# Optimization experiments

Measured on AMD Instinct MI355X. Metric: run time of the kernel, lower is better.

The kernel has to match this reference:

```python
import math
import jax, jax.numpy as jnp
import numpy as np

B, L, H = 32, 1024, 128

def setup_inputs() -> dict:
    key = jax.random.key(0)
    k1, k2, k3, k4 = jax.random.split(key, 4)
    a = jax.random.normal(k1, (B, L, H), dtype=jnp.float32)
    b = jax.random.normal(k2, (B, L, H), dtype=jnp.float32)
    mask_a = jax.random.randint(k3, (B, L, 1), 0, 2, dtype=jnp.int32)
    mask_b = jax.random.randint(k4, (B, L, 1), 0, 2, dtype=jnp.int32)
    temperature = jnp.asarray(1.0 / math.sqrt(H), dtype=jnp.float32)
    return {"a": a, "b": b, "mask_a": mask_a, "mask_b": mask_b, "temperature": temperature}

def reference(a, b, mask_a, mask_b, temperature):
    # scores: [B, La, Lb]
    scores = jnp.einsum('bld,bmd->blm', a, b) * temperature
    # outer product of token validity masks -> pair mask [B, La, Lb]
    mask = jnp.einsum('blk,bmk->blm', mask_a.astype(jnp.float32), mask_b.astype(jnp.float32)) > 0
    scores = jnp.where(mask, scores, jnp.float32(-10000.0))
    attention_a = jax.nn.softmax(scores, axis=1)  # normalize over La (columns)
    attention_b = jax.nn.softmax(scores, axis=2)  # normalize over Lb (rows)
    feature_a = jnp.einsum('blm,bmd->bld', attention_b, b)
    feature_b = jnp.einsum('blm,bmd->bld', attention_a, a)  # valid since La == Lb
    return (feature_a, feature_b)
```

## Files before the change

kernel.cpp:

```cpp
#include <hip/hip_runtime.h>
#include <math.h>

#define BN 32
#define LL 1024
#define HH 128

typedef __attribute__((ext_vector_type(8))) short short8;
typedef __attribute__((ext_vector_type(4))) float f32x4;

static const size_t SZ_BF = (size_t)BN * LL * HH * 2;

__device__ __forceinline__ ushort f2bf(float x) {
  union { float f; unsigned u; } c; c.f = x;
  unsigned r = c.u + 0x7fffu + ((c.u >> 16) & 1u);
  return (ushort)(r >> 16);
}
__device__ __forceinline__ float bf2f(ushort h) {
  union { unsigned u; float f; } c; c.u = ((unsigned)h) << 16;
  return c.f;
}
__device__ __forceinline__ short8 ld8(const ushort* p) {
  return *(const short8*)p;
}

__global__ __launch_bounds__(256) void k_convert(
    const float* __restrict__ a, const float* __restrict__ b,
    const int* __restrict__ mask_b,
    ushort* __restrict__ abf, ushort* __restrict__ bbf,
    ushort* __restrict__ aT, ushort* __restrict__ bT,
    float* __restrict__ meanb, float* __restrict__ invmean) {
  int bb = blockIdx.y;
  int l0 = blockIdx.x * 64;
  int which = blockIdx.z;
  const float* src = which ? b : a;
  ushort* dst  = which ? bbf : abf;
  ushort* dstT = which ? bT : aT;
  float* dmean = which ? meanb : invmean;
  __shared__ __align__(16) ushort T[128][72];
  __shared__ float accS[128];
  __shared__ float wgt[64];
  int t = threadIdx.x;
  if (t < 128) accS[t] = 0.f;
  if (t < 64)
    wgt[t] = which ? 1.0f : ((mask_b[bb * LL + l0 + t] == 0) ? 1.0f : 0.0f);
  int lrow = t >> 5;
  int dcol = (t & 31) * 4;
#pragma unroll
  for (int p = 0; p < 8; ++p) {
    int l = p * 8 + lrow;
    float4 v = *(const float4*)&src[((size_t)bb * LL + l0 + l) * HH + dcol];
    ushort4 u;
    u.x = f2bf(v.x); u.y = f2bf(v.y); u.z = f2bf(v.z); u.w = f2bf(v.w);
    *(ushort4*)&dst[((size_t)bb * LL + l0 + l) * HH + dcol] = u;
    T[dcol + 0][l] = u.x; T[dcol + 1][l] = u.y;
    T[dcol + 2][l] = u.z; T[dcol + 3][l] = u.w;
  }
  __syncthreads();
  int drow = t >> 3;
  int c8 = (t & 7) * 8;
#pragma unroll
  for (int q = 0; q < 4; ++q) {
    int d = q * 32 + drow;
    short8 val = *(const short8*)&T[d][c8];
    *(short8*)&dstT[((size_t)bb * HH + d) * LL + l0 + c8] = val;
    float s = 0.f;
#pragma unroll
    for (int j = 0; j < 8; ++j) s += wgt[c8 + j] * bf2f((ushort)val[j]);
    atomicAdd(&accS[d], s);
  }
  __syncthreads();
  if (t < 128) atomicAdd(&dmean[bb * HH + t], accS[t]);
}

__global__ __launch_bounds__(256, 2) void k_colsum(
    const ushort* __restrict__ abf, const ushort* __restrict__ bbf,
    const int* __restrict__ mask_a, const int* __restrict__ mask_b,
    const float* __restrict__ temp_p, float2* __restrict__ cc) {
  int bb = blockIdx.y;
  int m0 = blockIdx.x * 64;
  int t = threadIdx.x;
  int w = t >> 6, lane = t & 63, l16 = lane & 15, quad = lane >> 4;
  float temp = temp_p[0];
  __shared__ __align__(16) float biasA[LL];
  __shared__ float csred[4][4][16];
  for (int i = t; i < LL; i += 256)
    biasA[i] = mask_a[bb * LL + i] ? 0.0f : -10000.0f;

  short8 Bm[4][4];
  float biasB_mt[4];
#pragma unroll
  for (int mt = 0; mt < 4; ++mt) {
    int m = m0 + mt * 16 + l16;
    biasB_mt[mt] = mask_b[bb * LL + m] ? 0.0f : -10000.0f;
#pragma unroll
    for (int k = 0; k < 4; ++k)
      Bm[mt][k] = ld8(&bbf[((size_t)bb * LL + m) * HH + k * 32 + quad * 8]);
  }
  __syncthreads();

  float cs[4] = {0.f, 0.f, 0.f, 0.f};
  short8 Al0[4], Al1[4];

#define LOADAL(AlX, IT)                                                       \
  {                                                                           \
    const ushort* arow = &abf[((size_t)bb * LL + w * 256 + (IT) * 16 + l16) * HH]; \
    _Pragma("unroll") for (int k = 0; k < 4; ++k)                             \
        AlX[k] = ld8(&arow[k * 32 + quad * 8]);                               \
  }

#define CSCOMPUTE(AlX, IT)                                                    \
  {                                                                           \
    int lbase = w * 256 + (IT) * 16;                                          \
    f32x4 bA = *(const f32x4*)&biasA[lbase + quad * 4];                       \
    _Pragma("unroll") for (int mt = 0; mt < 4; ++mt) {                        \
      f32x4 sacc = {0.f, 0.f, 0.f, 0.f};                                      \
      _Pragma("unroll") for (int k = 0; k < 4; ++k)                           \
          sacc = __builtin_amdgcn_mfma_f32_16x16x32_bf16(AlX[k], Bm[mt][k],   \
                                                         sacc, 0, 0, 0);      \
      _Pragma("unroll") for (int r = 0; r < 4; ++r)                           \
          cs[mt] += __expf(sacc[r] * temp + bA[r] + biasB_mt[mt]);            \
    }                                                                         \
  }

  LOADAL(Al0, 0);
  for (int it = 0; it < 16; it += 2) {
    LOADAL(Al1, it + 1);
    CSCOMPUTE(Al0, it);
    LOADAL(Al0, (it + 2) & 15);
    CSCOMPUTE(Al1, it + 1);
  }
#undef LOADAL
#undef CSCOMPUTE

#pragma unroll
  for (int mt = 0; mt < 4; ++mt) {
    cs[mt] += __shfl_xor(cs[mt], 16);
    cs[mt] += __shfl_xor(cs[mt], 32);
  }
  if (lane < 16) {
#pragma unroll
    for (int mt = 0; mt < 4; ++mt) csred[w][mt][l16] = cs[mt];
  }
  __syncthreads();
  if (t < 64) {
    int mt = t >> 4, ml = t & 15;
    float s = csred[0][mt][ml] + csred[1][mt][ml] + csred[2][mt][ml] + csred[3][mt][ml];
    int m = m0 + t;
    float bB = mask_b[bb * LL + m] ? 0.0f : -10000.0f;
    cc[bb * LL + m] = make_float2(s > 0.f ? 1.0f / s : 0.0f, bB);
  }
}

__global__ __launch_bounds__(256, 2) void k_features(
    const ushort* __restrict__ abf, const ushort* __restrict__ bbf,
    const ushort* __restrict__ aT, const ushort* __restrict__ bT,
    const int* __restrict__ mask_a, const float* __restrict__ temp_p,
    const float2* __restrict__ cc, const float* __restrict__ meanb,
    const float* __restrict__ invmean, float* __restrict__ out) {
  int bb = blockIdx.y;
  int l0 = blockIdx.x * 64;
  int t = threadIdx.x;
  int w = t >> 6, lane = t & 63, l16 = lane & 15, quad = lane >> 4;
  float temp = temp_p[0];

  __shared__ float2 ccs[LL];
  __shared__ __align__(16) ushort Pa[2][64 * 72];
  __shared__ __align__(16) ushort Pb[2][64 * 72];
  __shared__ float rspart[4][64];
  __shared__ float rsfin[64];

  for (int i = t; i < LL; i += 256) ccs[i] = cc[bb * LL + i];

  float biasA_lt[4];
  short8 Afix[4][4];
#pragma unroll
  for (int lt = 0; lt < 4; ++lt) {
    int l = l0 + lt * 16 + l16;
    biasA_lt[lt] = mask_a[bb * LL + l] ? 0.0f : -10000.0f;
#pragma unroll
    for (int k = 0; k < 4; ++k)
      Afix[lt][k] = ld8(&abf[((size_t)bb * LL + l) * HH + k * 32 + quad * 8]);
  }

  f32x4 accA[4][2], accB[4][2];
  f32x4 zero = {0.f, 0.f, 0.f, 0.f};
#pragma unroll
  for (int lt = 0; lt < 4; ++lt)
#pragma unroll
    for (int dt = 0; dt < 2; ++dt) { accA[lt][dt] = zero; accB[lt][dt] = zero; }
  float rs_lt[4] = {0.f, 0.f, 0.f, 0.f};
  __syncthreads();

  short8 Am0[4], Am1[4];
  float2 cv0[4], cv1[4];
  short8 Bb[2][2], Ba[2][2];

#define LOADAM(AmX, cvX, M0)                                                  \
  {                                                                           \
    const ushort* brow = &bbf[((size_t)bb * LL + (M0) + w * 16 + l16) * HH];  \
    _Pragma("unroll") for (int k = 0; k < 4; ++k)                             \
        AmX[k] = ld8(&brow[k * 32 + quad * 8]);                               \
    _Pragma("unroll") for (int r = 0; r < 4; ++r)                             \
        cvX[r] = ccs[(M0) + w * 16 + quad * 4 + r];                           \
  }

#define LOADBT(M0)                                                            \
  {                                                                           \
    _Pragma("unroll") for (int dt = 0; dt < 2; ++dt) {                        \
      const ushort* btrow =                                                   \
          &bT[((size_t)bb * HH + w * 32 + dt * 16 + l16) * LL + (M0)];        \
      const ushort* atrow =                                                   \
          &aT[((size_t)bb * HH + w * 32 + dt * 16 + l16) * LL + (M0)];        \
      _Pragma("unroll") for (int ks = 0; ks < 2; ++ks) {                      \
        Bb[dt][ks] = ld8(&btrow[ks * 32 + quad * 8]);                         \
        Ba[dt][ks] = ld8(&atrow[ks * 32 + quad * 8]);                         \
      }                                                                       \
    }                                                                         \
  }

#define SPHASE(AmX, cvX)                                                      \
  {                                                                           \
    ushort* pa = &Pa[buf][0];                                                 \
    ushort* pb = &Pb[buf][0];                                                 \
    _Pragma("unroll") for (int lt = 0; lt < 4; ++lt) {                        \
      f32x4 sacc = zero;                                                      \
      _Pragma("unroll") for (int k = 0; k < 4; ++k)                           \
          sacc = __builtin_amdgcn_mfma_f32_16x16x32_bf16(AmX[k], Afix[lt][k], \
                                                         sacc, 0, 0, 0);      \
      ushort pav[4], pbv[4];                                                  \
      _Pragma("unroll") for (int r = 0; r < 4; ++r) {                         \
        float e = __expf(sacc[r] * temp + biasA_lt[lt] + cvX[r].y);           \
        pav[r] = f2bf(e);                                                     \
        rs_lt[lt] += bf2f(pav[r]);                                            \
        pbv[r] = f2bf(e * cvX[r].x);                                          \
      }                                                                       \
      uint2 ka, kb;                                                           \
      ka.x = (uint)pav[0] | ((uint)pav[1] << 16);                             \
      ka.y = (uint)pav[2] | ((uint)pav[3] << 16);                             \
      kb.x = (uint)pbv[0] | ((uint)pbv[1] << 16);                             \
      kb.y = (uint)pbv[2] | ((uint)pbv[3] << 16);                             \
      int pidx = (lt * 16 + l16) * 72 + w * 16 + quad * 4;                    \
      *(uint2*)&pa[pidx] = ka;                                                \
      *(uint2*)&pb[pidx] = kb;                                                \
    }                                                                         \
  }

#define FPHASE()                                                              \
  {                                                                           \
    const ushort* pa = &Pa[buf][0];                                           \
    const ushort* pb = &Pb[buf][0];                                           \
    _Pragma("unroll") for (int lt = 0; lt < 4; ++lt) {                        \
      _Pragma("unroll") for (int ks = 0; ks < 2; ++ks) {                      \
        int ridx = (lt * 16 + l16) * 72 + ks * 32 + quad * 8;                 \
        short8 PaF = *(const short8*)&pa[ridx];                               \
        short8 PbF = *(const short8*)&pb[ridx];                               \
        _Pragma("unroll") for (int dt = 0; dt < 2; ++dt) {                    \
          accA[lt][dt] = __builtin_amdgcn_mfma_f32_16x16x32_bf16(             \
              PaF, Bb[dt][ks], accA[lt][dt], 0, 0, 0);                        \
          accB[lt][dt] = __builtin_amdgcn_mfma_f32_16x16x32_bf16(             \
              PbF, Ba[dt][ks], accB[lt][dt], 0, 0, 0);                        \
        }                                                                     \
      }                                                                       \
    }                                                                         \
  }

  LOADAM(Am0, cv0, 0);
  int buf = 0;
  for (int m0 = 0; m0 < LL; m0 += 128) {
    LOADBT(m0);
    LOADAM(Am1, cv1, m0 + 64);
    SPHASE(Am0, cv0);
    __syncthreads();
    FPHASE();
    buf ^= 1;
    LOADBT(m0 + 64);
    LOADAM(Am0, cv0, (m0 + 128) & (LL - 1));
    SPHASE(Am1, cv1);
    __syncthreads();
    FPHASE();
    buf ^= 1;
  }
#undef LOADAM
#undef LOADBT
#undef SPHASE
#undef FPHASE

#pragma unroll
  for (int lt = 0; lt < 4; ++lt) {
    rs_lt[lt] += __shfl_xor(rs_lt[lt], 16);
    rs_lt[lt] += __shfl_xor(rs_lt[lt], 32);
  }
  if (lane < 16) {
#pragma unroll
    for (int lt = 0; lt < 4; ++lt) rspart[w][lt * 16 + l16] = rs_lt[lt];
  }
  __syncthreads();
  if (t < 64)
    rsfin[t] = rspart[0][t] + rspart[1][t] + rspart[2][t] + rspart[3][t];
  __syncthreads();

  float* outA = out;
  float* outB = out + (size_t)BN * LL * HH;
#pragma unroll
  for (int dt = 0; dt < 2; ++dt) {
    int d = w * 32 + dt * 16 + l16;
    float mb = meanb[bb * HH + d] * (1.0f / 1024.0f);
    float im = invmean[bb * HH + d] * (1.0f / 1024.0f);
#pragma unroll
    for (int lt = 0; lt < 4; ++lt) {
#pragma unroll
      for (int r = 0; r < 4; ++r) {
        int l = lt * 16 + quad * 4 + r;
        float rsv = rsfin[l];
        float fa = (rsv > 0.f) ? accA[lt][dt][r] / rsv : mb;
        float fb = accB[lt][dt][r] + im;
        outA[((size_t)bb * LL + l0 + l) * HH + d] = fa;
        outB[((size_t)bb * LL + l0 + l) * HH + d] = fb;
      }
    }
  }
}

extern "C" void kernel_launch(void* const* d_in, const int* in_sizes, int n_in,
                              void* d_out, int out_size, void* d_ws, size_t ws_size,
                              hipStream_t stream) {
  const float* a = (const float*)d_in[0];
  const float* b = (const float*)d_in[1];
  const int* mask_a = (const int*)d_in[2];
  const int* mask_b = (const int*)d_in[3];
  const float* temp = (const float*)d_in[4];
  float* out = (float*)d_out;

  char* wsb = (char*)d_ws;
  ushort* abf = (ushort*)(wsb + 0 * SZ_BF);
  ushort* bbf = (ushort*)(wsb + 1 * SZ_BF);
  ushort* aT  = (ushort*)(wsb + 2 * SZ_BF);
  ushort* bT  = (ushort*)(wsb + 3 * SZ_BF);
  float2* cc  = (float2*)(wsb + 4 * SZ_BF);
  float* meanb   = (float*)(wsb + 4 * SZ_BF + (size_t)BN * LL * sizeof(float2));
  float* invmean = meanb + BN * HH;

  hipMemsetAsync(meanb, 0, 2 * BN * HH * sizeof(float), stream);
  k_convert<<<dim3(16, 32, 2), 256, 0, stream>>>(a, b, mask_b, abf, bbf, aT, bT,
                                                 meanb, invmean);
  k_colsum<<<dim3(16, 32), 256, 0, stream>>>(abf, bbf, mask_a, mask_b, temp, cc);
  k_features<<<dim3(16, 32), 256, 0, stream>>>(abf, bbf, aT, bT, mask_a, temp,
                                               cc, meanb, invmean, out);
  (void)in_sizes; (void)n_in; (void)out_size; (void)ws_size;
}
```

Baseline: 206.7 us.

## Halve row tile to 32, move fixed A fragments to LDS, drop software prefetch

Both the column-sum and feature kernels now handle 32 rows per block instead of 64, doubling the grid to 1024 blocks and raising the launch-bounds occupancy hint from 2 to 4 waves per SIMD. In the feature kernel the fixed A fragments move from registers into shared memory, and the double-buffered register prefetch of B/A tiles is replaced by a simple per-iteration load. This cuts register pressure so more waves can hide latency. The cost is twice the re-reading of B and the transposed tiles across blocks, less MFMA work per load, and no explicit load/compute overlap.

```diff
diff --git a/kernel.cpp b/kernel.cpp
--- a/kernel.cpp
+++ b/kernel.cpp
@@ -72,24 +72,24 @@
   if (t < 128) atomicAdd(&dmean[bb * HH + t], accS[t]);
 }
 
-__global__ __launch_bounds__(256, 2) void k_colsum(
+__global__ __launch_bounds__(256, 4) void k_colsum(
     const ushort* __restrict__ abf, const ushort* __restrict__ bbf,
     const int* __restrict__ mask_a, const int* __restrict__ mask_b,
     const float* __restrict__ temp_p, float2* __restrict__ cc) {
   int bb = blockIdx.y;
-  int m0 = blockIdx.x * 64;
+  int m0 = blockIdx.x * 32;
   int t = threadIdx.x;
   int w = t >> 6, lane = t & 63, l16 = lane & 15, quad = lane >> 4;
   float temp = temp_p[0];
   __shared__ __align__(16) float biasA[LL];
-  __shared__ float csred[4][4][16];
+  __shared__ float csred[4][2][16];
   for (int i = t; i < LL; i += 256)
     biasA[i] = mask_a[bb * LL + i] ? 0.0f : -10000.0f;
 
-  short8 Bm[4][4];
-  float biasB_mt[4];
-#pragma unroll
-  for (int mt = 0; mt < 4; ++mt) {
+  short8 Bm[2][4];
+  float biasB_mt[2];
+#pragma unroll
+  for (int mt = 0; mt < 2; ++mt) {
     int m = m0 + mt * 16 + l16;
     biasB_mt[mt] = mask_b[bb * LL + m] ? 0.0f : -10000.0f;
 #pragma unroll
@@ -98,7 +98,7 @@
   }
   __syncthreads();
 
-  float cs[4] = {0.f, 0.f, 0.f, 0.f};
+  float cs[2] = {0.f, 0.f};
   short8 Al0[4], Al1[4];
 
 #define LOADAL(AlX, IT)                                                       \
@@ -112,7 +112,7 @@
   {                                                                           \
     int lbase = w * 256 + (IT) * 16;                                          \
     f32x4 bA = *(const f32x4*)&biasA[lbase + quad * 4];                       \
-    _Pragma("unroll") for (int mt = 0; mt < 4; ++mt) {                        \
+    _Pragma("unroll") for (int mt = 0; mt < 2; ++mt) {                        \
       f32x4 sacc = {0.f, 0.f, 0.f, 0.f};                                      \
       _Pragma("unroll") for (int k = 0; k < 4; ++k)                           \
           sacc = __builtin_amdgcn_mfma_f32_16x16x32_bf16(AlX[k], Bm[mt][k],   \
@@ -133,16 +133,16 @@
 #undef CSCOMPUTE
 
 #pragma unroll
-  for (int mt = 0; mt < 4; ++mt) {
+  for (int mt = 0; mt < 2; ++mt) {
     cs[mt] += __shfl_xor(cs[mt], 16);
     cs[mt] += __shfl_xor(cs[mt], 32);
   }
   if (lane < 16) {
 #pragma unroll
-    for (int mt = 0; mt < 4; ++mt) csred[w][mt][l16] = cs[mt];
-  }
-  __syncthreads();
-  if (t < 64) {
+    for (int mt = 0; mt < 2; ++mt) csred[w][mt][l16] = cs[mt];
+  }
+  __syncthreads();
+  if (t < 32) {
     int mt = t >> 4, ml = t & 15;
     float s = csred[0][mt][ml] + csred[1][mt][ml] + csred[2][mt][ml] + csred[3][mt][ml];
     int m = m0 + t;
@@ -151,151 +151,131 @@
   }
 }
 
-__global__ __launch_bounds__(256, 2) void k_features(
+__global__ __launch_bounds__(256, 4) void k_features(
     const ushort* __restrict__ abf, const ushort* __restrict__ bbf,
     const ushort* __restrict__ aT, const ushort* __restrict__ bT,
     const int* __restrict__ mask_a, const float* __restrict__ temp_p,
     const float2* __restrict__ cc, const float* __restrict__ meanb,
     const float* __restrict__ invmean, float* __restrict__ out) {
   int bb = blockIdx.y;
-  int l0 = blockIdx.x * 64;
+  int l0 = blockIdx.x * 32;
   int t = threadIdx.x;
   int w = t >> 6, lane = t & 63, l16 = lane & 15, quad = lane >> 4;
   float temp = temp_p[0];
 
   __shared__ float2 ccs[LL];
-  __shared__ __align__(16) ushort Pa[2][64 * 72];
-  __shared__ __align__(16) ushort Pb[2][64 * 72];
-  __shared__ float rspart[4][64];
-  __shared__ float rsfin[64];
+  __shared__ __align__(16) ushort Pa[2][32 * 72];
+  __shared__ __align__(16) ushort Pb[2][32 * 72];
+  __shared__ short8 AfixS[512];
+  __shared__ float rspart[4][32];
+  __shared__ float rsfin[32];
 
   for (int i = t; i < LL; i += 256) ccs[i] = cc[bb * LL + i];
 
-  float biasA_lt[4];
-  short8 Afix[4][4];
-#pragma unroll
-  for (int lt = 0; lt < 4; ++lt) {
+  {
+    int l16p = t & 15, quadp = (t >> 4) & 3, kp = t >> 6;
+#pragma unroll
+    for (int lt = 0; lt < 2; ++lt) {
+      short8 v = ld8(&abf[((size_t)bb * LL + l0 + lt * 16 + l16p) * HH +
+                          kp * 32 + quadp * 8]);
+      AfixS[((lt * 4 + kp) * 4 + quadp) * 16 + l16p] = v;
+    }
+  }
+
+  float biasA_lt[2];
+#pragma unroll
+  for (int lt = 0; lt < 2; ++lt) {
     int l = l0 + lt * 16 + l16;
     biasA_lt[lt] = mask_a[bb * LL + l] ? 0.0f : -10000.0f;
-#pragma unroll
-    for (int k = 0; k < 4; ++k)
-      Afix[lt][k] = ld8(&abf[((size_t)bb * LL + l) * HH + k * 32 + quad * 8]);
-  }
-
-  f32x4 accA[4][2], accB[4][2];
+  }
+
+  f32x4 accA[2][2], accB[2][2];
   f32x4 zero = {0.f, 0.f, 0.f, 0.f};
 #pragma unroll
-  for (int lt = 0; lt < 4; ++lt)
+  for (int lt = 0; lt < 2; ++lt)
 #pragma unroll
     for (int dt = 0; dt < 2; ++dt) { accA[lt][dt] = zero; accB[lt][dt] = zero; }
-  float rs_lt[4] = {0.f, 0.f, 0.f, 0.f};
-  __syncthreads();
-
-  short8 Am0[4], Am1[4];
-  float2 cv0[4], cv1[4];
-  short8 Bb[2][2], Ba[2][2];
-
-#define LOADAM(AmX, cvX, M0)                                                  \
-  {                                                                           \
-    const ushort* brow = &bbf[((size_t)bb * LL + (M0) + w * 16 + l16) * HH];  \
-    _Pragma("unroll") for (int k = 0; k < 4; ++k)                             \
-        AmX[k] = ld8(&brow[k * 32 + quad * 8]);                               \
-    _Pragma("unroll") for (int r = 0; r < 4; ++r)                             \
-        cvX[r] = ccs[(M0) + w * 16 + quad * 4 + r];                           \
-  }
-
-#define LOADBT(M0)                                                            \
-  {                                                                           \
-    _Pragma("unroll") for (int dt = 0; dt < 2; ++dt) {                        \
-      const ushort* btrow =                                                   \
-          &bT[((size_t)bb * HH + w * 32 + dt * 16 + l16) * LL + (M0)];        \
-      const ushort* atrow =                                                   \
-          &aT[((size_t)bb * HH + w * 32 + dt * 16 + l16) * LL + (M0)];        \
-      _Pragma("unroll") for (int ks = 0; ks < 2; ++ks) {                      \
-        Bb[dt][ks] = ld8(&btrow[ks * 32 + quad * 8]);                         \
-        Ba[dt][ks] = ld8(&atrow[ks * 32 + quad * 8]);                         \
-      }                                                                       \
-    }                                                                         \
-  }
-
-#define SPHASE(AmX, cvX)                                                      \
-  {                                                                           \
-    ushort* pa = &Pa[buf][0];                                                 \
-    ushort* pb = &Pb[buf][0];                                                 \
-    _Pragma("unroll") for (int lt = 0; lt < 4; ++lt) {                        \
-      f32x4 sacc = zero;                                                      \
-      _Pragma("unroll") for (int k = 0; k < 4; ++k)                           \
-          sacc = __builtin_amdgcn_mfma_f32_16x16x32_bf16(AmX[k], Afix[lt][k], \
-                                                         sacc, 0, 0, 0);      \
-      ushort pav[4], pbv[4];                                                  \
-      _Pragma("unroll") for (int r = 0; r < 4; ++r) {                         \
-        float e = __expf(sacc[r] * temp + biasA_lt[lt] + cvX[r].y);           \
-        pav[r] = f2bf(e);                                                     \
-        rs_lt[lt] += bf2f(pav[r]);                                            \
-        pbv[r] = f2bf(e * cvX[r].x);                                          \
-      }                                                                       \
-      uint2 ka, kb;                                                           \
-      ka.x = (uint)pav[0] | ((uint)pav[1] << 16);                             \
-      ka.y = (uint)pav[2] | ((uint)pav[3] << 16);                             \
-      kb.x = (uint)pbv[0] | ((uint)pbv[1] << 16);                             \
-      kb.y = (uint)pbv[2] | ((uint)pbv[3] << 16);                             \
-      int pidx = (lt * 16 + l16) * 72 + w * 16 + quad * 4;                    \
-      *(uint2*)&pa[pidx] = ka;                                                \
-      *(uint2*)&pb[pidx] = kb;                                                \
-    }                                                                         \
-  }
-
-#define FPHASE()                                                              \
-  {                                                                           \
-    const ushort* pa = &Pa[buf][0];                                           \
-    const ushort* pb = &Pb[buf][0];                                           \
-    _Pragma("unroll") for (int lt = 0; lt < 4; ++lt) {                        \
-      _Pragma("unroll") for (int ks = 0; ks < 2; ++ks) {                      \
-        int ridx = (lt * 16 + l16) * 72 + ks * 32 + quad * 8;                 \
-        short8 PaF = *(const short8*)&pa[ridx];                               \
-        short8 PbF = *(const short8*)&pb[ridx];                               \
-        _Pragma("unroll") for (int dt = 0; dt < 2; ++dt) {                    \
-          accA[lt][dt] = __builtin_amdgcn_mfma_f32_16x16x32_bf16(             \
-              PaF, Bb[dt][ks], accA[lt][dt], 0, 0, 0);                        \
-          accB[lt][dt] = __builtin_amdgcn_mfma_f32_16x16x32_bf16(             \
-              PbF, Ba[dt][ks], accB[lt][dt], 0, 0, 0);                        \
-        }                                                                     \
-      }                                                                       \
-    }                                                                         \
-  }
-
-  LOADAM(Am0, cv0, 0);
+  float rs_lt[2] = {0.f, 0.f};
+  __syncthreads();
+
   int buf = 0;
-  for (int m0 = 0; m0 < LL; m0 += 128) {
-    LOADBT(m0);
-    LOADAM(Am1, cv1, m0 + 64);
-    SPHASE(Am0, cv0);
+  for (int mq = 0; mq < LL; mq += 64) {
+    short8 Am[4];
+    const ushort* brow = &bbf[((size_t)bb * LL + mq + w * 16 + l16) * HH];
+#pragma unroll
+    for (int k = 0; k < 4; ++k) Am[k] = ld8(&brow[k * 32 + quad * 8]);
+    short8 Bb[2][2], Ba[2][2];
+#pragma unroll
+    for (int dt = 0; dt < 2; ++dt) {
+      const ushort* btrow = &bT[((size_t)bb * HH + w * 32 + dt * 16 + l16) * LL + mq];
+      const ushort* atrow = &aT[((size_t)bb * HH + w * 32 + dt * 16 + l16) * LL + mq];
+#pragma unroll
+      for (int ks = 0; ks < 2; ++ks) {
+        Bb[dt][ks] = ld8(&btrow[ks * 32 + quad * 8]);
+        Ba[dt][ks] = ld8(&atrow[ks * 32 + quad * 8]);
+      }
+    }
+    float2 cv[4];
+#pragma unroll
+    for (int r = 0; r < 4; ++r) cv[r] = ccs[mq + w * 16 + quad * 4 + r];
+
+    ushort* pa = &Pa[buf][0];
+    ushort* pb = &Pb[buf][0];
+#pragma unroll
+    for (int lt = 0; lt < 2; ++lt) {
+      f32x4 sacc = zero;
+#pragma unroll
+      for (int k = 0; k < 4; ++k) {
+        short8 af = AfixS[((lt * 4 + k) * 4 + quad) * 16 + l16];
+        sacc = __builtin_amdgcn_mfma_f32_16x16x32_bf16(Am[k], af, sacc, 0, 0, 0);
+      }
+      ushort pav[4], pbv[4];
+#pragma unroll
+      for (int r = 0; r < 4; ++r) {
+        float e = __expf(sacc[r] * temp + biasA_lt[lt] + cv[r].y);
+        pav[r] = f2bf(e);
+        rs_lt[lt] += bf2f(pav[r]);
+        pbv[r] = f2bf(e * cv[r].x);
+      }
+      uint2 ka, kb;
+      ka.x = (uint)pav[0] | ((uint)pav[1] << 16);
+      ka.y = (uint)pav[2] | ((uint)pav[3] << 16);
+      kb.x = (uint)pbv[0] | ((uint)pbv[1] << 16);
+      kb.y = (uint)pbv[2] | ((uint)pbv[3] << 16);
+      int pidx = (lt * 16 + l16) * 72 + w * 16 + quad * 4;
+      *(uint2*)&pa[pidx] = ka;
+      *(uint2*)&pb[pidx] = kb;
+    }
     __syncthreads();
-    FPHASE();
+
+#pragma unroll
+    for (int lt = 0; lt < 2; ++lt) {
+#pragma unroll
+      for (int ks = 0; ks < 2; ++ks) {
+        int ridx = (lt * 16 + l16) * 72 + ks * 32 + quad * 8;
+        short8 PaF = *(const short8*)&pa[ridx];
+        short8 PbF = *(const short8*)&pb[ridx];
+#pragma unroll
+        for (int dt = 0; dt < 2; ++dt) {
+          accA[lt][dt] = __builtin_amdgcn_mfma_f32_16x16x32_bf16(PaF, Bb[dt][ks], accA[lt][dt], 0, 0, 0);
+          accB[lt][dt] = __builtin_amdgcn_mfma_f32_16x16x32_bf16(PbF, Ba[dt][ks], accB[lt][dt], 0, 0, 0);
+        }
+      }
+    }
     buf ^= 1;
-    LOADBT(m0 + 64);
-    LOADAM(Am0, cv0, (m0 + 128) & (LL - 1));
-    SPHASE(Am1, cv1);
-    __syncthreads();
-    FPHASE();
-    buf ^= 1;
-  }
-#undef LOADAM
-#undef LOADBT
-#undef SPHASE
-#undef FPHASE
-
-#pragma unroll
-  for (int lt = 0; lt < 4; ++lt) {
+  }
+
+#pragma unroll
+  for (int lt = 0; lt < 2; ++lt) {
     rs_lt[lt] += __shfl_xor(rs_lt[lt], 16);
     rs_lt[lt] += __shfl_xor(rs_lt[lt], 32);
   }
   if (lane < 16) {
 #pragma unroll
-    for (int lt = 0; lt < 4; ++lt) rspart[w][lt * 16 + l16] = rs_lt[lt];
-  }
-  __syncthreads();
-  if (t < 64)
+    for (int lt = 0; lt < 2; ++lt) rspart[w][lt * 16 + l16] = rs_lt[lt];
+  }
+  __syncthreads();
+  if (t < 32)
     rsfin[t] = rspart[0][t] + rspart[1][t] + rspart[2][t] + rspart[3][t];
   __syncthreads();
 
@@ -307,7 +287,7 @@
     float mb = meanb[bb * HH + d] * (1.0f / 1024.0f);
     float im = invmean[bb * HH + d] * (1.0f / 1024.0f);
 #pragma unroll
-    for (int lt = 0; lt < 4; ++lt) {
+    for (int lt = 0; lt < 2; ++lt) {
 #pragma unroll
       for (int r = 0; r < 4; ++r) {
         int l = lt * 16 + quad * 4 + r;
@@ -343,8 +323,8 @@
   hipMemsetAsync(meanb, 0, 2 * BN * HH * sizeof(float), stream);
   k_convert<<<dim3(16, 32, 2), 256, 0, stream>>>(a, b, mask_b, abf, bbf, aT, bT,
                                                  meanb, invmean);
-  k_colsum<<<dim3(16, 32), 256, 0, stream>>>(abf, bbf, mask_a, mask_b, temp, cc);
-  k_features<<<dim3(16, 32), 256, 0, stream>>>(abf, bbf, aT, bT, mask_a, temp,
+  k_colsum<<<dim3(32, 32), 256, 0, stream>>>(abf, bbf, mask_a, mask_b, temp, cc);
+  k_features<<<dim3(32, 32), 256, 0, stream>>>(abf, bbf, aT, bT, mask_a, temp,
                                                cc, meanb, invmean, out);
   (void)in_sizes; (void)n_in; (void)out_size; (void)ws_size;
 }
```

New measurement: 228.8 us. +10.7%, slower.
